# Performance work log

Measured on AMD Instinct MI355X. Metric: run time of the kernel, lower is better.

The kernel has to match this reference:

```python
import jax, jax.numpy as jnp
import numpy as np

C, DFF, NH, NL, NP_, Q, B = 256, 1024, 8, 4, 4, 300, 8
SHAPES = [(128, 128), (64, 64), (32, 32), (16, 16)]  # (H_l, W_l) per level
S = sum(h * w for h, w in SHAPES)  # 21760 flattened multi-scale tokens
DH = C // NH
EPS = 1e-5


def _ln(x, g, b):
    m = x.mean(-1, keepdims=True)
    v = jnp.var(x, axis=-1, keepdims=True)
    return (x - m) / jnp.sqrt(v + EPS) * g + b


def _bilinear(value_l, loc, Hl, Wl):
    # value_l: [B,NH,Hl*Wl,DH]; loc: [B,Q,NH,P,2] normalized to [0,1]
    # torch grid_sample(align_corners=False, padding='zeros') with grid=2*loc-1
    Bb, Qq, nh, P, _ = loc.shape
    x = loc[..., 0] * Wl - 0.5
    y = loc[..., 1] * Hl - 0.5
    x0 = jnp.floor(x)
    y0 = jnp.floor(y)
    wx = x - x0
    wy = y - y0
    out = jnp.zeros((Bb, nh, Qq * P, value_l.shape[-1]), value_l.dtype)
    for dy in (0, 1):
        for dx in (0, 1):
            xi = x0 + dx
            yi = y0 + dy
            w = (wx if dx else 1.0 - wx) * (wy if dy else 1.0 - wy)
            valid = (xi >= 0) & (xi < Wl) & (yi >= 0) & (yi < Hl)
            idx = (jnp.clip(yi, 0, Hl - 1) * Wl + jnp.clip(xi, 0, Wl - 1)).astype(jnp.int32)
            idx = idx.transpose(0, 2, 1, 3).reshape(Bb, nh, Qq * P)
            v = jnp.take_along_axis(value_l, idx[..., None], axis=2)  # [B,NH,QP,DH]
            wz = jnp.where(valid, w, 0.0).transpose(0, 2, 1, 3).reshape(Bb, nh, Qq * P)
            out = out + v * wz[..., None]
    return out.reshape(Bb, nh, Qq, P, -1)


def setup_inputs() -> dict:
    key = jax.random.key(0)
    ks = iter(jax.random.split(key, 48))
    rn = lambda shape, s=1.0: jax.random.normal(next(ks), shape, jnp.float32) * s
    p = {}
    p['tgt'] = rn((B, Q, C))
    p['tgt_box'] = rn((B, Q, C))  # unused on this branch (online=False), kept for signature parity
    p['query_pos'] = rn((B, Q, C))
    p['reference_points'] = jax.random.uniform(next(ks), (B, 1, Q, NL, 2), jnp.float32)
    p['src'] = rn((B, S, C))
    p['spatial_shapes'] = jnp.array(SHAPES, jnp.int32)
    p['level_start_index'] = jnp.array(np.cumsum([0] + [h * w for h, w in SHAPES[:-1]]), jnp.int32)
    p['src_padding_mask'] = jnp.zeros((B, S), bool)
    dims = dict(wq=(C, C), wk=(C, C), wv=(C, C), wo=(C, C),
                w_off=(NH * NL * NP_ * 2, C), w_attn=(NH * NL * NP_, C),
                w_val=(C, C), w_out=(C, C), w1=(DFF, C), w2=(C, DFF))
    for n, (o, i) in dims.items():
        p[n] = rn((o, i), 0.02)
        p[n.replace('w', 'b', 1)] = jnp.zeros((o,), jnp.float32)
    for n in ('ln2', 'ln1', 'ln3'):
        p[n + '_g'] = jnp.ones((C,), jnp.float32)
        p[n + '_b'] = jnp.zeros((C,), jnp.float32)
    return p


def reference(tgt, tgt_box, query_pos, reference_points, src, spatial_shapes,
              level_start_index, src_padding_mask,
              wq, bq, wk, bk, wv, bv, wo, bo,
              w_off, b_off, w_attn, b_attn, w_val, b_val, w_out, b_out,
              w1, b1, w2, b2, ln2_g, ln2_b, ln1_g, ln1_b, ln3_g, ln3_b):
    # ---- self attention (nn.MultiheadAttention, q=k=tgt+pos, v=tgt) ----
    q = tgt + query_pos
    qh = (q @ wq.T + bq).reshape(B, Q, NH, DH)
    kh = (q @ wk.T + bk).reshape(B, Q, NH, DH)
    vh = (tgt @ wv.T + bv).reshape(B, Q, NH, DH)
    logits = jnp.einsum('bqhd,bkhd->bhqk', qh, kh) / np.float32(np.sqrt(DH))
    a = jax.nn.softmax(logits, axis=-1)
    sa = jnp.einsum('bhqk,bkhd->bqhd', a, vh).reshape(B, Q, C) @ wo.T + bo
    tgt = _ln(tgt + sa, ln2_g, ln2_b)
    # ---- multi-scale deformable cross attention (MSDeformAttn) ----
    query = tgt + query_pos
    value = src @ w_val.T + b_val
    value = jnp.where(src_padding_mask[..., None], 0.0, value)
    value = value.reshape(B, S, NH, DH).transpose(0, 2, 1, 3)  # [B,NH,S,DH]
    off = (query @ w_off.T + b_off).reshape(B, Q, NH, NL, NP_, 2)
    aw = jax.nn.softmax((query @ w_attn.T + b_attn).reshape(B, Q, NH, NL * NP_), axis=-1)
    aw = aw.reshape(B, Q, NH, NL, NP_)
    offset_norm = jnp.array([[wl, hl] for hl, wl in SHAPES], jnp.float32)  # [NL,2] = (W,H)
    ref = reference_points[:, 0]  # frame axis nf=1 -> [B,Q,NL,2]
    loc = ref[:, :, None, :, None, :] + off / offset_norm[None, None, None, :, None, :]
    starts = np.cumsum([0] + [h * w for h, w in SHAPES])
    acc = jnp.zeros((B, NH, Q, DH), jnp.float32)
    for l, (hl, wl) in enumerate(SHAPES):
        vl = value[:, :, starts[l]:starts[l + 1], :]
        samp = _bilinear(vl, loc[:, :, :, l], hl, wl)  # [B,NH,Q,P,DH]
        acc = acc + jnp.einsum('bhqpd,bqhp->bhqd', samp, aw[:, :, :, l])
    tgt2 = acc.transpose(0, 2, 1, 3).reshape(B, Q, C) @ w_out.T + b_out
    tgt = _ln(tgt + tgt2, ln1_g, ln1_b)
    # ---- FFN (box branch) ----
    ff = jax.nn.relu(tgt @ w1.T + b1) @ w2.T + b2
    tgt = _ln(tgt + ff, ln3_g, ln3_b)
    return tgt[:, None]  # matches torch tgt.unsqueeze(1): [B,1,Q,C]
```

## Files before the change

### kernel.cpp

```cpp
#include <hip/hip_runtime.h>
#include <hip/hip_bf16.h>
#include <math.h>

#define Bb   8
#define Qq   300
#define Cc   256
#define NHh  8
#define DHh  32
#define Ss   21760
#define DFFf 1024
#define LN_EPS 1e-5f

typedef __hip_bfloat16 bf16;
typedef unsigned short u16;
typedef unsigned int u32;
typedef __bf16 bf16x8_t __attribute__((ext_vector_type(8)));
typedef __bf16 bf16x4_t __attribute__((ext_vector_type(4)));
typedef float f32x4_t __attribute__((ext_vector_type(4)));

__device__ inline u16 f2bf(float f) {
  union { float f; u32 u; } v; v.f = f;
  u32 u = v.u + 0x7fffu + ((v.u >> 16) & 1u);
  return (u16)(u >> 16);
}
__device__ inline float bfbits_lo(u32 w) {
  union { u32 u; float f; } v; v.u = w << 16;
  return v.f;
}
__device__ inline float bfbits_hi(u32 w) {
  union { u32 u; float f; } v; v.u = w & 0xffff0000u;
  return v.f;
}

__device__ inline __bf16* lds_bf16(__bf16* base, int row, int chunk, int sub) {
  return base + (row << 8) + (((chunk ^ (row & 7)) << 3) + sub);
}

#define FR_WQ    0
#define FR_WK    128
#define FR_WV    256
#define FR_WO    384
#define FR_WVAL  512
#define FR_WOFF  640
#define FR_WATTN 768
#define FR_WOUT  832
#define FR_W1    960
#define FR_W2    1472
#define FR_TOTAL 1984

#define VGRID 2720
#define AGRID 1216
#define TGRID 3936

__global__ __launch_bounds__(256) void pack_weights(
    const float* __restrict__ wq, const float* __restrict__ wk,
    const float* __restrict__ wv, const float* __restrict__ wo,
    const float* __restrict__ wval, const float* __restrict__ woff,
    const float* __restrict__ wattn, const float* __restrict__ wout,
    const float* __restrict__ w1, const float* __restrict__ w2,
    __bf16* __restrict__ Bpk)
{
  const int gw = (int)((blockIdx.x * blockDim.x + threadIdx.x) >> 6);
  const int lane = threadIdx.x & 63;
  if (gw >= FR_TOTAL) return;
  const float* W; int KT, base;
  if      (gw < FR_WK)   { W = wq;    KT = 8;  base = FR_WQ; }
  else if (gw < FR_WV)   { W = wk;    KT = 8;  base = FR_WK; }
  else if (gw < FR_WO)   { W = wv;    KT = 8;  base = FR_WV; }
  else if (gw < FR_WVAL) { W = wo;    KT = 8;  base = FR_WO; }
  else if (gw < FR_WOFF) { W = wval;  KT = 8;  base = FR_WVAL; }
  else if (gw < FR_WATTN){ W = woff;  KT = 8;  base = FR_WOFF; }
  else if (gw < FR_WOUT) { W = wattn; KT = 8;  base = FR_WATTN; }
  else if (gw < FR_W1)   { W = wout;  KT = 8;  base = FR_WOUT; }
  else if (gw < FR_W2)   { W = w1;    KT = 8;  base = FR_W1; }
  else                   { W = w2;    KT = 32; base = FR_W2; }
  const int f = gw - base;
  const int nf = f / KT, kt = f % KT;
  const int col = nf * 16 + (lane & 15);
  const int k0 = kt * 32 + (lane >> 4) * 8;
  const int K = KT * 32;
  const float4 a = *reinterpret_cast<const float4*>(W + (size_t)col * K + k0);
  const float4 b = *reinterpret_cast<const float4*>(W + (size_t)col * K + k0 + 4);
  bf16x8_t p = { (__bf16)a.x, (__bf16)a.y, (__bf16)a.z, (__bf16)a.w,
                 (__bf16)b.x, (__bf16)b.y, (__bf16)b.z, (__bf16)b.w };
  *reinterpret_cast<bf16x8_t*>(Bpk + ((size_t)gw * 64 + lane) * 8) = p;
}

template<int KT, bool RELU>
__device__ __forceinline__ void gemmS_body(
    __bf16* As,
    const float* __restrict__ A, const float* __restrict__ A2,
    const __bf16* __restrict__ Wp, const float* __restrict__ bias,
    float* __restrict__ out, int M, int N, int m0, int n0)
{
  const int tid = threadIdx.x;
  const int w = tid >> 6, lane = tid & 63;
  const int wm = w >> 1, wn = w & 1;
  const int fr = lane & 15, fq = lane >> 4;
  constexpr int K = KT * 32;

  float bld[4];
  #pragma unroll
  for (int n = 0; n < 4; ++n) bld[n] = bias[n0 + wn * 64 + n * 16 + fr];

  f32x4_t acc[2][4];
  const f32x4_t zz = {0.f, 0.f, 0.f, 0.f};
  #pragma unroll
  for (int m = 0; m < 2; ++m)
    #pragma unroll
    for (int n = 0; n < 4; ++n) acc[m][n] = zz;

  #pragma unroll
  for (int kc = 0; kc < KT / 8; ++kc) {
    if (kc) __syncthreads();
    #pragma unroll
    for (int rnd = 0; rnd < 2; ++rnd) {
      float4 pa[8];
      #pragma unroll
      for (int j = 0; j < 8; ++j) {
        const int row = m0 + w * 16 + rnd * 8 + j;
        const int ar = (row < M) ? row : (M - 1);
        pa[j] = *reinterpret_cast<const float4*>(A + (size_t)ar * K + kc * 256 + lane * 4);
        if (A2) {
          const float4 c = *reinterpret_cast<const float4*>(A2 + (size_t)ar * K + kc * 256 + lane * 4);
          pa[j].x += c.x; pa[j].y += c.y; pa[j].z += c.z; pa[j].w += c.w;
        }
      }
      #pragma unroll
      for (int j = 0; j < 8; ++j)
        *reinterpret_cast<bf16x4_t*>(lds_bf16(As, w * 16 + rnd * 8 + j, lane >> 1, (lane & 1) * 4)) =
            bf16x4_t{ (__bf16)pa[j].x, (__bf16)pa[j].y, (__bf16)pa[j].z, (__bf16)pa[j].w };
    }
    __syncthreads();
    #pragma unroll
    for (int kt2 = 0; kt2 < 8; ++kt2) {
      const int kt = kc * 8 + kt2;
      bf16x8_t bfr[4];
      #pragma unroll
      for (int n = 0; n < 4; ++n)
        bfr[n] = *reinterpret_cast<const bf16x8_t*>(
            Wp + (size_t)(((n0 >> 4) + wn * 4 + n) * KT + kt) * 512 + (size_t)lane * 8);
      bf16x8_t af[2];
      #pragma unroll
      for (int m = 0; m < 2; ++m)
        af[m] = *reinterpret_cast<const bf16x8_t*>(
            lds_bf16(As, wm * 32 + m * 16 + fr, kt2 * 4 + fq, 0));
      #pragma unroll
      for (int m = 0; m < 2; ++m)
        #pragma unroll
        for (int n = 0; n < 4; ++n)
          acc[m][n] = __builtin_amdgcn_mfma_f32_16x16x32_bf16(af[m], bfr[n], acc[m][n], 0, 0, 0);
    }
  }

  #pragma unroll
  for (int m = 0; m < 2; ++m) {
    const int row = m0 + wm * 32 + m * 16 + fq * 4;
    #pragma unroll
    for (int n = 0; n < 4; ++n) {
      const int col = n0 + wn * 64 + n * 16 + fr;
      #pragma unroll
      for (int j = 0; j < 4; ++j) {
        if (row + j < M) {
          float v = acc[m][n][j] + bld[n];
          if (RELU) v = fmaxf(v, 0.f);
          out[(size_t)(row + j) * N + col] = v;
        }
      }
    }
  }
}

template<int KT, bool RELU>
__global__ __launch_bounds__(256) void gemm64(
    const float* __restrict__ A, const float* __restrict__ A2,
    const __bf16* __restrict__ Wp, const float* __restrict__ bias,
    float* __restrict__ out, int M, int N)
{
  __shared__ __bf16 As[64 * 256];
  gemmS_body<KT, RELU>(As, A, A2, Wp, bias, out, M, N, blockIdx.y * 64, blockIdx.x * 128);
}

__global__ __launch_bounds__(256) void gemm_qkv(
    const float* __restrict__ tgt, const float* __restrict__ qpos,
    const __bf16* __restrict__ Bpk,
    const float* __restrict__ bq, const float* __restrict__ bk, const float* __restrict__ bv,
    float* __restrict__ qhb, float* __restrict__ khb, float* __restrict__ vhb, int M)
{
  __shared__ __bf16 As[64 * 256];
  const int sel = blockIdx.x >> 1;
  const int n0 = (blockIdx.x & 1) * 128;
  const __bf16* Wp; const float* bias; float* out; const float* A2;
  if (sel == 0)      { Wp = Bpk + (size_t)FR_WQ * 512; bias = bq; out = qhb; A2 = qpos; }
  else if (sel == 1) { Wp = Bpk + (size_t)FR_WK * 512; bias = bk; out = khb; A2 = qpos; }
  else               { Wp = Bpk + (size_t)FR_WV * 512; bias = bv; out = vhb; A2 = nullptr; }
  gemmS_body<8, false>(As, tgt, A2, Wp, bias, out, M, 256, blockIdx.y * 64, n0);
}

__global__ __launch_bounds__(256) void gemm_offattn(
    const float* __restrict__ tgt1, const float* __restrict__ qpos,
    const __bf16* __restrict__ Bpk,
    const float* __restrict__ b_off, const float* __restrict__ b_attn,
    float* __restrict__ offb, float* __restrict__ awlb, int M)
{
  __shared__ __bf16 As[64 * 256];
  const int bx = blockIdx.x;
  if (bx < 2)
    gemmS_body<8, false>(As, tgt1, qpos, Bpk + (size_t)FR_WOFF * 512, b_off, offb,
                         M, 256, blockIdx.y * 64, bx * 128);
  else
    gemmS_body<8, false>(As, tgt1, qpos, Bpk + (size_t)FR_WATTN * 512, b_attn, awlb,
                         M, 128, blockIdx.y * 64, 0);
}

template<int KT>
__global__ __launch_bounds__(256) void gemm_ln(
    const float* __restrict__ A, const __bf16* __restrict__ Wp,
    const float* __restrict__ bias, const float* __restrict__ X,
    const float* __restrict__ g, const float* __restrict__ beta,
    float* __restrict__ out, int M)
{
  __shared__ __bf16 As[64 * 256];
  __shared__ float R[64][260];
  const int tid = threadIdx.x;
  const int w = tid >> 6, lane = tid & 63;
  const int wm = w >> 1, wn = w & 1;
  const int fr = lane & 15, fq = lane >> 4;
  const int m0 = blockIdx.x * 64;
  constexpr int K = KT * 32;

  float bld[8];
  #pragma unroll
  for (int n = 0; n < 8; ++n) bld[n] = bias[wn * 128 + n * 16 + fr];

  f32x4_t acc[2][8];
  const f32x4_t zz = {0.f, 0.f, 0.f, 0.f};
  #pragma unroll
  for (int m = 0; m < 2; ++m)
    #pragma unroll
    for (int n = 0; n < 8; ++n) acc[m][n] = zz;

  #pragma unroll
  for (int kc = 0; kc < KT / 8; ++kc) {
    if (kc) __syncthreads();
    #pragma unroll
    for (int rnd = 0; rnd < 2; ++rnd) {
      float4 pa[8];
      #pragma unroll
      for (int j = 0; j < 8; ++j) {
        const int row = m0 + w * 16 + rnd * 8 + j;
        const int ar = (row < M) ? row : (M - 1);
        pa[j] = *reinterpret_cast<const float4*>(A + (size_t)ar * K + kc * 256 + lane * 4);
      }
      #pragma unroll
      for (int j = 0; j < 8; ++j)
        *reinterpret_cast<bf16x4_t*>(lds_bf16(As, w * 16 + rnd * 8 + j, lane >> 1, (lane & 1) * 4)) =
            bf16x4_t{ (__bf16)pa[j].x, (__bf16)pa[j].y, (__bf16)pa[j].z, (__bf16)pa[j].w };
    }
    __syncthreads();
    #pragma unroll
    for (int kt2 = 0; kt2 < 8; ++kt2) {
      const int kt = kc * 8 + kt2;
      bf16x8_t bfr[8];
      #pragma unroll
      for (int n = 0; n < 8; ++n)
        bfr[n] = *reinterpret_cast<const bf16x8_t*>(
            Wp + (size_t)((wn * 8 + n) * KT + kt) * 512 + (size_t)lane * 8);
      bf16x8_t af[2];
      #pragma unroll
      for (int m = 0; m < 2; ++m)
        af[m] = *reinterpret_cast<const bf16x8_t*>(
            lds_bf16(As, wm * 32 + m * 16 + fr, kt2 * 4 + fq, 0));
      #pragma unroll
      for (int m = 0; m < 2; ++m)
        #pragma unroll
        for (int n = 0; n < 8; ++n)
          acc[m][n] = __builtin_amdgcn_mfma_f32_16x16x32_bf16(af[m], bfr[n], acc[m][n], 0, 0, 0);
    }
  }

  #pragma unroll
  for (int m = 0; m < 2; ++m)
    #pragma unroll
    for (int n = 0; n < 8; ++n)
      #pragma unroll
      for (int j = 0; j < 4; ++j)
        R[wm * 32 + m * 16 + fq * 4 + j][wn * 128 + n * 16 + fr] = acc[m][n][j] + bld[n];
  __syncthreads();

  const int r = tid >> 2, p = tid & 3;
  const int grow = m0 + r;
  const int ar = (grow < M) ? grow : (M - 1);
  float4 vbuf[16];
  float sum = 0.f, sq = 0.f;
  #pragma unroll
  for (int i = 0; i < 16; ++i) {
    float4 v = *reinterpret_cast<const float4*>(&R[r][p * 64 + i * 4]);
    const float4 x = *reinterpret_cast<const float4*>(X + (size_t)ar * 256 + p * 64 + i * 4);
    v.x += x.x; v.y += x.y; v.z += x.z; v.w += x.w;
    vbuf[i] = v;
    sum += v.x + v.y + v.z + v.w;
    sq += v.x * v.x + v.y * v.y + v.z * v.z + v.w * v.w;
  }
  sum += __shfl_xor(sum, 1); sum += __shfl_xor(sum, 2);
  sq  += __shfl_xor(sq, 1);  sq  += __shfl_xor(sq, 2);
  const float mean = sum * (1.f / 256.f);
  const float var = sq * (1.f / 256.f) - mean * mean;
  const float sc = rsqrtf(var + LN_EPS);
  if (grow < M) {
    #pragma unroll
    for (int i = 0; i < 16; ++i) {
      const float4 gg = *reinterpret_cast<const float4*>(g + p * 64 + i * 4);
      const float4 bb = *reinterpret_cast<const float4*>(beta + p * 64 + i * 4);
      float4 o;
      o.x = (vbuf[i].x - mean) * sc * gg.x + bb.x;
      o.y = (vbuf[i].y - mean) * sc * gg.y + bb.y;
      o.z = (vbuf[i].z - mean) * sc * gg.z + bb.z;
      o.w = (vbuf[i].w - mean) * sc * gg.w + bb.w;
      *reinterpret_cast<float4*>(out + (size_t)grow * 256 + p * 64 + i * 4) = o;
    }
  }
}

struct AttnSh { u16 Kb[304][38]; u16 Vb[304][36]; float pbuf[4][304]; };
struct ValSh  { __bf16 As[64 * 256]; };

__global__ __launch_bounds__(256, 3) void val_attn(
    const float* __restrict__ src, const __bf16* __restrict__ Bpk,
    const float* __restrict__ b_val, bf16* __restrict__ valb,
    const float* __restrict__ qh, const float* __restrict__ kh,
    const float* __restrict__ vh, float* __restrict__ sa)
{
  __shared__ union { AttnSh a; ValSh v; } sh;
  const int tid = threadIdx.x;
  const int w = tid >> 6, lane = tid & 63;
  const int fr = lane & 15, fq = lane >> 4;

  const int bid = blockIdx.x;
  const bool is_attn = (bid < 3648) && (bid % 3 == 2);
  const int wid = is_attn ? (bid / 3)
                          : (bid < 3648 ? (bid / 3) * 2 + (bid % 3) : bid - AGRID);

  if (!is_attn) {
    __bf16* As = sh.v.As;
    const __bf16* Wp = Bpk + (size_t)FR_WVAL * 512;
    const size_t m0 = (size_t)wid * 64;

    float bld[4];
    #pragma unroll
    for (int n = 0; n < 4; ++n) bld[n] = b_val[w * 64 + n * 16 + fr];

    const float* g = src + (m0 + (size_t)w * 16) * 256 + lane * 4;
    float4 p[16];
    #pragma unroll
    for (int j = 0; j < 16; ++j)
      p[j] = *reinterpret_cast<const float4*>(g + (size_t)j * 256);
    #pragma unroll
    for (int j = 0; j < 16; ++j)
      *reinterpret_cast<bf16x4_t*>(lds_bf16(As, w * 16 + j, lane >> 1, (lane & 1) * 4)) =
          bf16x4_t{ (__bf16)p[j].x, (__bf16)p[j].y, (__bf16)p[j].z, (__bf16)p[j].w };

    f32x4_t acc[4][4];
    const f32x4_t zz = {0.f, 0.f, 0.f, 0.f};
    #pragma unroll
    for (int m = 0; m < 4; ++m)
      #pragma unroll
      for (int n = 0; n < 4; ++n) acc[m][n] = zz;

    const __bf16* wpl = Wp + (size_t)lane * 8;
    __syncthreads();

    #pragma unroll
    for (int kt = 0; kt < 8; ++kt) {
      bf16x8_t bfr[4];
      #pragma unroll
      for (int n = 0; n < 4; ++n)
        bfr[n] = *reinterpret_cast<const bf16x8_t*>(wpl + (size_t)((w * 4 + n) * 8 + kt) * 512);
      bf16x8_t af[4];
      #pragma unroll
      for (int m = 0; m < 4; ++m)
        af[m] = *reinterpret_cast<const bf16x8_t*>(
            lds_bf16(As, m * 16 + fr, kt * 4 + fq, 0));
      #pragma unroll
      for (int m = 0; m < 4; ++m)
        #pragma unroll
        for (int n = 0; n < 4; ++n)
          acc[m][n] = __builtin_amdgcn_mfma_f32_16x16x32_bf16(af[m], bfr[n], acc[m][n], 0, 0, 0);
    }

    __syncthreads();
    #pragma unroll
    for (int m = 0; m < 4; ++m)
      #pragma unroll
      for (int n = 0; n < 4; ++n)
        #pragma unroll
        for (int j = 0; j < 4; ++j)
          *lds_bf16(As, m * 16 + fq * 4 + j, w * 8 + n * 2 + (fr >> 3), fr & 7) =
              (__bf16)(acc[m][n][j] + bld[n]);
    __syncthreads();
    #pragma unroll
    for (int i = 0; i < 8; ++i) {
      const int pby = i * 4096 + tid * 16;
      const int row = pby >> 9;
      const int chunk = (pby & 511) >> 4;
      const bf16x8_t v = *reinterpret_cast<const bf16x8_t*>(lds_bf16(As, row, chunk, 0));
      *reinterpret_cast<bf16x8_t*>(
          reinterpret_cast<char*>(valb + (m0 + row) * 256) + (pby & 511)) = v;
    }
    return;
  }

  auto& Kb = sh.a.Kb;
  auto& Vb = sh.a.Vb;
  auto& pbuf = sh.a.pbuf;
  const int qt = wid % 19;
  const int bh = wid / 19;
  const int h = bh & 7, b = bh >> 3;
  const size_t base = ((size_t)b * Qq) * Cc + h * DHh;

  for (int idx = tid; idx < 304 * 16; idx += 256) {
    const int k = idx >> 4, dd = idx & 15;
    u32 kw = 0, vw = 0;
    if (k < Qq) {
      const float2 kf = *reinterpret_cast<const float2*>(kh + base + (size_t)k * Cc + 2 * dd);
      const float2 vf = *reinterpret_cast<const float2*>(vh + base + (size_t)k * Cc + 2 * dd);
      kw = (u32)f2bf(kf.x * 0.17677669529663687f) |
           ((u32)f2bf(kf.y * 0.17677669529663687f) << 16);
      vw = (u32)f2bf(vf.x) | ((u32)f2bf(vf.y) << 16);
    }
    *reinterpret_cast<u32*>(&Kb[k][2 * dd]) = kw;
    *reinterpret_cast<u32*>(&Vb[k][2 * dd]) = vw;
  }
  __syncthreads();

  const int qtr = lane >> 4, dp = lane & 15;

  for (int r = 0; r < 4; ++r) {
    const int q0 = qt * 16 + w * 4 + r;
    const int q = (q0 < Qq) ? q0 : (Qq - 1);
    const float* qp = qh + base + (size_t)q * Cc;
    float qv[32];
    #pragma unroll
    for (int i = 0; i < 8; ++i) {
      const float4 t = reinterpret_cast<const float4*>(qp)[i];
      qv[i*4+0] = t.x; qv[i*4+1] = t.y; qv[i*4+2] = t.z; qv[i*4+3] = t.w;
    }

    float e[5];
    float mx = -1e30f;
    #pragma unroll
    for (int i = 0; i < 5; ++i) {
      const int k = lane + i * 64;
      if (k < Qq) {
        const u32* kp = reinterpret_cast<const u32*>(&Kb[k][0]);
        float s = 0.f;
        #pragma unroll
        for (int d2 = 0; d2 < 16; ++d2) {
          const u32 kw = kp[d2];
          s = fmaf(qv[2*d2], bfbits_lo(kw), s);
          s = fmaf(qv[2*d2+1], bfbits_hi(kw), s);
        }
        e[i] = s;
      } else {
        e[i] = -1e30f;
      }
      mx = fmaxf(mx, e[i]);
    }
    #pragma unroll
    for (int o = 32; o; o >>= 1) mx = fmaxf(mx, __shfl_xor(mx, o));
    float ssum = 0.f;
    #pragma unroll
    for (int i = 0; i < 5; ++i) { e[i] = __expf(e[i] - mx); ssum += e[i]; }
    #pragma unroll
    for (int o = 32; o; o >>= 1) ssum += __shfl_xor(ssum, o);
    const float inv = 1.f / ssum;
    #pragma unroll
    for (int i = 0; i < 5; ++i) {
      const int k = lane + i * 64;
      if (k < 304) pbuf[w][k] = (k < Qq) ? e[i] * inv : 0.f;
    }
    __syncthreads();

    float accA = 0.f, accB = 0.f;
    const float* prow = pbuf[w] + qtr * 76;
    #pragma unroll 4
    for (int j4 = 0; j4 < 19; ++j4) {
      const float4 pv4 = *reinterpret_cast<const float4*>(prow + j4 * 4);
      const int kb = qtr * 76 + j4 * 4;
      const u32 v0 = *reinterpret_cast<const u32*>(&Vb[kb + 0][2*dp]);
      const u32 v1 = *reinterpret_cast<const u32*>(&Vb[kb + 1][2*dp]);
      const u32 v2 = *reinterpret_cast<const u32*>(&Vb[kb + 2][2*dp]);
      const u32 v3 = *reinterpret_cast<const u32*>(&Vb[kb + 3][2*dp]);
      accA = fmaf(pv4.x, bfbits_lo(v0), accA); accB = fmaf(pv4.x, bfbits_hi(v0), accB);
      accA = fmaf(pv4.y, bfbits_lo(v1), accA); accB = fmaf(pv4.y, bfbits_hi(v1), accB);
      accA = fmaf(pv4.z, bfbits_lo(v2), accA); accB = fmaf(pv4.z, bfbits_hi(v2), accB);
      accA = fmaf(pv4.w, bfbits_lo(v3), accA); accB = fmaf(pv4.w, bfbits_hi(v3), accB);
    }
    accA += __shfl_xor(accA, 16); accA += __shfl_xor(accA, 32);
    accB += __shfl_xor(accB, 16); accB += __shfl_xor(accB, 32);
    if (q0 < Qq && lane < 16) {
      float2 st; st.x = accA; st.y = accB;
      *reinterpret_cast<float2*>(sa + base + (size_t)q * Cc + 2 * dp) = st;
    }
    __syncthreads();
  }
}

__global__ __launch_bounds__(256) void deform_kernel(
    const float* __restrict__ offb, const float* __restrict__ awl,
    const float* __restrict__ refp, const bf16* __restrict__ value,
    float* __restrict__ accp)
{
  const int gw = (int)((blockIdx.x * (size_t)blockDim.x + threadIdx.x) >> 6);
  if (gw >= Bb * Qq * NHh) return;
  const int lane = threadIdx.x & 63;
  const int h = gw % NHh;
  const int t = gw / NHh;
  const int qi = t % Qq;
  const int b = t / Qq;
  const int pt = lane >> 4;
  const int dp = lane & 15;

  const float* awp = awl + (size_t)(b * Qq + qi) * 128 + h * 16;
  float e[16];
  float mx = -1e30f;
  #pragma unroll
  for (int i = 0; i < 16; ++i) { e[i] = awp[i]; mx = fmaxf(mx, e[i]); }
  float s = 0.f;
  #pragma unroll
  for (int i = 0; i < 16; ++i) { e[i] = __expf(e[i] - mx); s += e[i]; }
  const float inv = 1.f / s;

  const float* offp = offb + (size_t)(b * Qq + qi) * Cc + h * 32;
  const float* rp = refp + (size_t)(b * Qq + qi) * 8;
  const int lH[4] = {128, 64, 32, 16};
  const int lW[4] = {128, 64, 32, 16};
  const int lS[4] = {0, 16384, 20480, 21504};

  const u16* vbase = reinterpret_cast<const u16*>(value) + (size_t)h * 32 + 2 * dp;

  float accx = 0.f, accy = 0.f;
  #pragma unroll
  for (int l = 0; l < 4; ++l) {
    const int Hl = lH[l], Wl = lW[l], st = lS[l];
    const float rx = rp[l * 2 + 0], ry = rp[l * 2 + 1];
    const float ax = offp[l * 8 + pt * 2 + 0];
    const float ay = offp[l * 8 + pt * 2 + 1];
    const float x = (rx + ax / (float)Wl) * (float)Wl - 0.5f;
    const float y = (ry + ay / (float)Hl) * (float)Hl - 0.5f;
    const float x0f = floorf(x), y0f = floorf(y);
    const float wx = x - x0f, wy = y - y0f;
    const int x0 = (int)x0f, y0 = (int)y0f;
    const float wp = e[l * 4 + pt] * inv;
    #pragma unroll
    for (int dy = 0; dy < 2; ++dy) {
      #pragma unroll
      for (int dx = 0; dx < 2; ++dx) {
        const int xi = x0 + dx, yi = y0 + dy;
        if (xi >= 0 && xi < Wl && yi >= 0 && yi < Hl) {
          const float wgt = wp * (dx ? wx : 1.f - wx) * (dy ? wy : 1.f - wy);
          const u32 v = *reinterpret_cast<const u32*>(
              vbase + (size_t)(b * (size_t)Ss + st + yi * Wl + xi) * Cc);
          accx = fmaf(wgt, bfbits_lo(v), accx);
          accy = fmaf(wgt, bfbits_hi(v), accy);
        }
      }
    }
  }
  accx += __shfl_xor(accx, 16); accx += __shfl_xor(accx, 32);
  accy += __shfl_xor(accy, 16); accy += __shfl_xor(accy, 32);
  if (lane < 16) {
    float2 st2; st2.x = accx; st2.y = accy;
    *reinterpret_cast<float2*>(accp + (size_t)(b * Qq + qi) * Cc + h * 32 + 2 * dp) = st2;
  }
}

extern "C" void kernel_launch(void* const* d_in, const int* in_sizes, int n_in,
                              void* d_out, int out_size, void* d_ws, size_t ws_size,
                              hipStream_t stream) {
  const float* tgt   = (const float*)d_in[0];
  const float* qpos  = (const float*)d_in[2];
  const float* refp  = (const float*)d_in[3];
  const float* src   = (const float*)d_in[4];
  const float* wq = (const float*)d_in[8];   const float* bq = (const float*)d_in[9];
  const float* wk = (const float*)d_in[10];  const float* bk = (const float*)d_in[11];
  const float* wv = (const float*)d_in[12];  const float* bv = (const float*)d_in[13];
  const float* wo = (const float*)d_in[14];  const float* bo = (const float*)d_in[15];
  const float* w_off = (const float*)d_in[16];  const float* b_off = (const float*)d_in[17];
  const float* w_attn = (const float*)d_in[18]; const float* b_attn = (const float*)d_in[19];
  const float* w_val = (const float*)d_in[20];  const float* b_val = (const float*)d_in[21];
  const float* w_out = (const float*)d_in[22];  const float* b_out = (const float*)d_in[23];
  const float* w1 = (const float*)d_in[24];  const float* b1 = (const float*)d_in[25];
  const float* w2 = (const float*)d_in[26];  const float* b2 = (const float*)d_in[27];
  const float* ln2g = (const float*)d_in[28]; const float* ln2b = (const float*)d_in[29];
  const float* ln1g = (const float*)d_in[30]; const float* ln1b = (const float*)d_in[31];
  const float* ln3g = (const float*)d_in[32]; const float* ln3b = (const float*)d_in[33];

  float* fws = (float*)d_ws;
  const size_t NBQ = (size_t)Bb * Qq * Cc;
  float* qhb  = fws;
  float* khb  = qhb  + NBQ;
  float* vhb  = khb  + NBQ;
  float* sab  = vhb  + NBQ;
  float* tgt1 = sab  + NBQ;
  float* offb = tgt1 + NBQ;
  float* accb = offb + NBQ;
  float* t2nb = accb + NBQ;
  float* awlb = t2nb + NBQ;
  float* ffhb = awlb + (size_t)Bb * Qq * 128;
  bf16*  valb = (bf16*)(ffhb + (size_t)Bb * Qq * DFFf);
  __bf16* Bpk = (__bf16*)(valb + (size_t)Bb * Ss * Cc);

  const int MQ = Bb * Qq;
  const int MT = (MQ + 63) / 64;
  dim3 blk(256, 1, 1);

  pack_weights<<<dim3((FR_TOTAL + 3) / 4), blk, 0, stream>>>(
      wq, wk, wv, wo, w_val, w_off, w_attn, w_out, w1, w2, Bpk);

  gemm_qkv<<<dim3(6, MT), blk, 0, stream>>>(tgt, qpos, Bpk, bq, bk, bv, qhb, khb, vhb, MQ);

  val_attn<<<dim3(TGRID), blk, 0, stream>>>(
      src, Bpk, b_val, valb, qhb, khb, vhb, sab);

  gemm_ln<8><<<dim3(MT), blk, 0, stream>>>(
      sab, Bpk + (size_t)FR_WO * 512, bo, tgt, ln2g, ln2b, tgt1, MQ);

  gemm_offattn<<<dim3(3, MT), blk, 0, stream>>>(tgt1, qpos, Bpk, b_off, b_attn, offb, awlb, MQ);

  deform_kernel<<<dim3(Bb * Qq * NHh / 4), blk, 0, stream>>>(offb, awlb, refp, valb, accb);

  gemm_ln<8><<<dim3(MT), blk, 0, stream>>>(
      accb, Bpk + (size_t)FR_WOUT * 512, b_out, tgt1, ln1g, ln1b, t2nb, MQ);

  gemm64<8, true><<<dim3(8, MT), blk, 0, stream>>>(t2nb, nullptr, Bpk + (size_t)FR_W1 * 512, b1, ffhb, MQ, DFFf);
  gemm_ln<32><<<dim3(MT), blk, 0, stream>>>(
      ffhb, Bpk + (size_t)FR_W2 * 512, b2, t2nb, ln3g, ln3b, (float*)d_out, MQ);
}
```

Baseline: 208.4 us.

## Halve gemm_ln row tile and read self-attn V from global instead of LDS

The fused GEMM+LayerNorm kernel now processes 32 rows per block instead of 64, so it launches twice as many blocks over the 2400-row problem and uses less shared memory and fewer accumulators per block. The self-attention path stops staging V in LDS and reads fp32 V directly from global memory (clamped indices), shrinking shared memory so val_attn can request higher occupancy (launch bounds 3→5). The trade-offs are that each block re-reads the weight tile for only half as many rows, and V reads are now uncoalesced global loads rather than LDS hits. Using fp32 V instead of bf16 also changes precision slightly.

```diff
diff --git a/kernel.cpp b/kernel.cpp
--- a/kernel.cpp
+++ b/kernel.cpp
@@ -220,41 +220,38 @@
     const float* __restrict__ g, const float* __restrict__ beta,
     float* __restrict__ out, int M)
 {
-  __shared__ __bf16 As[64 * 256];
-  __shared__ float R[64][260];
+  __shared__ __bf16 As[32 * 256];
+  __shared__ float R[32][260];
   const int tid = threadIdx.x;
   const int w = tid >> 6, lane = tid & 63;
   const int wm = w >> 1, wn = w & 1;
   const int fr = lane & 15, fq = lane >> 4;
-  const int m0 = blockIdx.x * 64;
+  const int m0 = blockIdx.x * 32;
   constexpr int K = KT * 32;
 
   float bld[8];
   #pragma unroll
   for (int n = 0; n < 8; ++n) bld[n] = bias[wn * 128 + n * 16 + fr];
 
-  f32x4_t acc[2][8];
+  f32x4_t acc[8];
   const f32x4_t zz = {0.f, 0.f, 0.f, 0.f};
   #pragma unroll
-  for (int m = 0; m < 2; ++m)
-    #pragma unroll
-    for (int n = 0; n < 8; ++n) acc[m][n] = zz;
+  for (int n = 0; n < 8; ++n) acc[n] = zz;
 
   #pragma unroll
   for (int kc = 0; kc < KT / 8; ++kc) {
     if (kc) __syncthreads();
-    #pragma unroll
-    for (int rnd = 0; rnd < 2; ++rnd) {
+    {
       float4 pa[8];
       #pragma unroll
       for (int j = 0; j < 8; ++j) {
-        const int row = m0 + w * 16 + rnd * 8 + j;
+        const int row = m0 + w * 8 + j;
         const int ar = (row < M) ? row : (M - 1);
         pa[j] = *reinterpret_cast<const float4*>(A + (size_t)ar * K + kc * 256 + lane * 4);
       }
       #pragma unroll
       for (int j = 0; j < 8; ++j)
-        *reinterpret_cast<bf16x4_t*>(lds_bf16(As, w * 16 + rnd * 8 + j, lane >> 1, (lane & 1) * 4)) =
+        *reinterpret_cast<bf16x4_t*>(lds_bf16(As, w * 8 + j, lane >> 1, (lane & 1) * 4)) =
             bf16x4_t{ (__bf16)pa[j].x, (__bf16)pa[j].y, (__bf16)pa[j].z, (__bf16)pa[j].w };
     }
     __syncthreads();
@@ -266,66 +263,59 @@
       for (int n = 0; n < 8; ++n)
         bfr[n] = *reinterpret_cast<const bf16x8_t*>(
             Wp + (size_t)((wn * 8 + n) * KT + kt) * 512 + (size_t)lane * 8);
-      bf16x8_t af[2];
-      #pragma unroll
-      for (int m = 0; m < 2; ++m)
-        af[m] = *reinterpret_cast<const bf16x8_t*>(
-            lds_bf16(As, wm * 32 + m * 16 + fr, kt2 * 4 + fq, 0));
-      #pragma unroll
-      for (int m = 0; m < 2; ++m)
-        #pragma unroll
-        for (int n = 0; n < 8; ++n)
-          acc[m][n] = __builtin_amdgcn_mfma_f32_16x16x32_bf16(af[m], bfr[n], acc[m][n], 0, 0, 0);
-    }
-  }
-
-  #pragma unroll
-  for (int m = 0; m < 2; ++m)
-    #pragma unroll
-    for (int n = 0; n < 8; ++n)
-      #pragma unroll
-      for (int j = 0; j < 4; ++j)
-        R[wm * 32 + m * 16 + fq * 4 + j][wn * 128 + n * 16 + fr] = acc[m][n][j] + bld[n];
+      const bf16x8_t af = *reinterpret_cast<const bf16x8_t*>(
+          lds_bf16(As, wm * 16 + fr, kt2 * 4 + fq, 0));
+      #pragma unroll
+      for (int n = 0; n < 8; ++n)
+        acc[n] = __builtin_amdgcn_mfma_f32_16x16x32_bf16(af, bfr[n], acc[n], 0, 0, 0);
+    }
+  }
+
+  #pragma unroll
+  for (int n = 0; n < 8; ++n)
+    #pragma unroll
+    for (int j = 0; j < 4; ++j)
+      R[wm * 16 + fq * 4 + j][wn * 128 + n * 16 + fr] = acc[n][j] + bld[n];
   __syncthreads();
 
-  const int r = tid >> 2, p = tid & 3;
+  const int r = tid >> 3, p = tid & 7;
   const int grow = m0 + r;
   const int ar = (grow < M) ? grow : (M - 1);
-  float4 vbuf[16];
+  float4 vbuf[8];
   float sum = 0.f, sq = 0.f;
   #pragma unroll
-  for (int i = 0; i < 16; ++i) {
-    float4 v = *reinterpret_cast<const float4*>(&R[r][p * 64 + i * 4]);
-    const float4 x = *reinterpret_cast<const float4*>(X + (size_t)ar * 256 + p * 64 + i * 4);
+  for (int i = 0; i < 8; ++i) {
+    float4 v = *reinterpret_cast<const float4*>(&R[r][p * 32 + i * 4]);
+    const float4 x = *reinterpret_cast<const float4*>(X + (size_t)ar * 256 + p * 32 + i * 4);
     v.x += x.x; v.y += x.y; v.z += x.z; v.w += x.w;
     vbuf[i] = v;
     sum += v.x + v.y + v.z + v.w;
     sq += v.x * v.x + v.y * v.y + v.z * v.z + v.w * v.w;
   }
-  sum += __shfl_xor(sum, 1); sum += __shfl_xor(sum, 2);
-  sq  += __shfl_xor(sq, 1);  sq  += __shfl_xor(sq, 2);
+  sum += __shfl_xor(sum, 1); sum += __shfl_xor(sum, 2); sum += __shfl_xor(sum, 4);
+  sq  += __shfl_xor(sq, 1);  sq  += __shfl_xor(sq, 2);  sq  += __shfl_xor(sq, 4);
   const float mean = sum * (1.f / 256.f);
   const float var = sq * (1.f / 256.f) - mean * mean;
   const float sc = rsqrtf(var + LN_EPS);
   if (grow < M) {
     #pragma unroll
-    for (int i = 0; i < 16; ++i) {
-      const float4 gg = *reinterpret_cast<const float4*>(g + p * 64 + i * 4);
-      const float4 bb = *reinterpret_cast<const float4*>(beta + p * 64 + i * 4);
+    for (int i = 0; i < 8; ++i) {
+      const float4 gg = *reinterpret_cast<const float4*>(g + p * 32 + i * 4);
+      const float4 bb = *reinterpret_cast<const float4*>(beta + p * 32 + i * 4);
       float4 o;
       o.x = (vbuf[i].x - mean) * sc * gg.x + bb.x;
       o.y = (vbuf[i].y - mean) * sc * gg.y + bb.y;
       o.z = (vbuf[i].z - mean) * sc * gg.z + bb.z;
       o.w = (vbuf[i].w - mean) * sc * gg.w + bb.w;
-      *reinterpret_cast<float4*>(out + (size_t)grow * 256 + p * 64 + i * 4) = o;
-    }
-  }
-}
-
-struct AttnSh { u16 Kb[304][38]; u16 Vb[304][36]; float pbuf[4][304]; };
+      *reinterpret_cast<float4*>(out + (size_t)grow * 256 + p * 32 + i * 4) = o;
+    }
+  }
+}
+
+struct AttnSh { u16 Kb[304][38]; float pbuf[4][304]; };
 struct ValSh  { __bf16 As[64 * 256]; };
 
-__global__ __launch_bounds__(256, 3) void val_attn(
+__global__ __launch_bounds__(256, 5) void val_attn(
     const float* __restrict__ src, const __bf16* __restrict__ Bpk,
     const float* __restrict__ b_val, bf16* __restrict__ valb,
     const float* __restrict__ qh, const float* __restrict__ kh,
@@ -411,7 +401,6 @@
   }
 
   auto& Kb = sh.a.Kb;
-  auto& Vb = sh.a.Vb;
   auto& pbuf = sh.a.pbuf;
   const int qt = wid % 19;
   const int bh = wid / 19;
@@ -420,20 +409,18 @@
 
   for (int idx = tid; idx < 304 * 16; idx += 256) {
     const int k = idx >> 4, dd = idx & 15;
-    u32 kw = 0, vw = 0;
+    u32 kw = 0;
     if (k < Qq) {
       const float2 kf = *reinterpret_cast<const float2*>(kh + base + (size_t)k * Cc + 2 * dd);
-      const float2 vf = *reinterpret_cast<const float2*>(vh + base + (size_t)k * Cc + 2 * dd);
       kw = (u32)f2bf(kf.x * 0.17677669529663687f) |
            ((u32)f2bf(kf.y * 0.17677669529663687f) << 16);
-      vw = (u32)f2bf(vf.x) | ((u32)f2bf(vf.y) << 16);
     }
     *reinterpret_cast<u32*>(&Kb[k][2 * dd]) = kw;
-    *reinterpret_cast<u32*>(&Vb[k][2 * dd]) = vw;
   }
   __syncthreads();
 
   const int qtr = lane >> 4, dp = lane & 15;
+  const float* vrow = vh + base + 2 * dp;
 
   for (int r = 0; r < 4; ++r) {
     const int q0 = qt * 16 + w * 4 + r;
@@ -487,14 +474,18 @@
     for (int j4 = 0; j4 < 19; ++j4) {
       const float4 pv4 = *reinterpret_cast<const float4*>(prow + j4 * 4);
       const int kb = qtr * 76 + j4 * 4;
-      const u32 v0 = *reinterpret_cast<const u32*>(&Vb[kb + 0][2*dp]);
-      const u32 v1 = *reinterpret_cast<const u32*>(&Vb[kb + 1][2*dp]);
-      const u32 v2 = *reinterpret_cast<const u32*>(&Vb[kb + 2][2*dp]);
-      const u32 v3 = *reinterpret_cast<const u32*>(&Vb[kb + 3][2*dp]);
-      accA = fmaf(pv4.x, bfbits_lo(v0), accA); accB = fmaf(pv4.x, bfbits_hi(v0), accB);
-      accA = fmaf(pv4.y, bfbits_lo(v1), accA); accB = fmaf(pv4.y, bfbits_hi(v1), accB);
-      accA = fmaf(pv4.z, bfbits_lo(v2), accA); accB = fmaf(pv4.z, bfbits_hi(v2), accB);
-      accA = fmaf(pv4.w, bfbits_lo(v3), accA); accB = fmaf(pv4.w, bfbits_hi(v3), accB);
+      const int k0 = (kb + 0 < Qq) ? kb + 0 : (Qq - 1);
+      const int k1 = (kb + 1 < Qq) ? kb + 1 : (Qq - 1);
+      const int k2 = (kb + 2 < Qq) ? kb + 2 : (Qq - 1);
+      const int k3 = (kb + 3 < Qq) ? kb + 3 : (Qq - 1);
+      const float2 v0 = *reinterpret_cast<const float2*>(vrow + (size_t)k0 * Cc);
+      const float2 v1 = *reinterpret_cast<const float2*>(vrow + (size_t)k1 * Cc);
+      const float2 v2 = *reinterpret_cast<const float2*>(vrow + (size_t)k2 * Cc);
+      const float2 v3 = *reinterpret_cast<const float2*>(vrow + (size_t)k3 * Cc);
+      accA = fmaf(pv4.x, v0.x, accA); accB = fmaf(pv4.x, v0.y, accB);
+      accA = fmaf(pv4.y, v1.x, accA); accB = fmaf(pv4.y, v1.y, accB);
+      accA = fmaf(pv4.z, v2.x, accA); accB = fmaf(pv4.z, v2.y, accB);
+      accA = fmaf(pv4.w, v3.x, accA); accB = fmaf(pv4.w, v3.y, accB);
     }
     accA += __shfl_xor(accA, 16); accA += __shfl_xor(accA, 32);
     accB += __shfl_xor(accB, 16); accB += __shfl_xor(accB, 32);
@@ -613,6 +604,7 @@
 
   const int MQ = Bb * Qq;
   const int MT = (MQ + 63) / 64;
+  const int MT2 = (MQ + 31) / 32;
   dim3 blk(256, 1, 1);
 
   pack_weights<<<dim3((FR_TOTAL + 3) / 4), blk, 0, stream>>>(
@@ -623,17 +615,17 @@
   val_attn<<<dim3(TGRID), blk, 0, stream>>>(
       src, Bpk, b_val, valb, qhb, khb, vhb, sab);
 
-  gemm_ln<8><<<dim3(MT), blk, 0, stream>>>(
+  gemm_ln<8><<<dim3(MT2), blk, 0, stream>>>(
       sab, Bpk + (size_t)FR_WO * 512, bo, tgt, ln2g, ln2b, tgt1, MQ);
 
   gemm_offattn<<<dim3(3, MT), blk, 0, stream>>>(tgt1, qpos, Bpk, b_off, b_attn, offb, awlb, MQ);
 
   deform_kernel<<<dim3(Bb * Qq * NHh / 4), blk, 0, stream>>>(offb, awlb, refp, valb, accb);
 
-  gemm_ln<8><<<dim3(MT), blk, 0, stream>>>(
+  gemm_ln<8><<<dim3(MT2), blk, 0, stream>>>(
       accb, Bpk + (size_t)FR_WOUT * 512, b_out, tgt1, ln1g, ln1b, t2nb, MQ);
 
   gemm64<8, true><<<dim3(8, MT), blk, 0, stream>>>(t2nb, nullptr, Bpk + (size_t)FR_W1 * 512, b1, ffhb, MQ, DFFf);
-  gemm_ln<32><<<dim3(MT), blk, 0, stream>>>(
+  gemm_ln<32><<<dim3(MT2), blk, 0, stream>>>(
       ffhb, Bpk + (size_t)FR_W2 * 512, b2, t2nb, ln3g, ln3b, (float*)d_out, MQ);
 }
```

Result: slower. 313.0 us (+50.2%).
